# Performance work log

Measured on AMD Instinct MI355X. Metric: run time of the kernel, lower is better.

## Reference

```python
import jax, jax.numpy as jnp
import numpy as np

PI = 3.141592653589793

def _rel_transform(ent, rel):
    # ent: [E, d], rel: [E, d/2] (RotatE-style rotation composition)
    re, im = jnp.split(ent, 2, axis=-1)
    r = rel / (1.5 / PI)
    cr, sr = jnp.cos(r), jnp.sin(r)
    return jnp.concatenate([re * cr + im * sr, re * sr - im * cr], axis=-1)

def setup_inputs() -> dict:
    key = jax.random.key(0)
    ks = jax.random.split(key, 10)
    num_ent, d, num_rel, E2 = 100000, 128, 500, 1000000
    def kaiming(k, shape):
        fan_in = shape[1] if len(shape) > 1 else shape[0]
        return jax.random.normal(k, shape, jnp.float32) * np.sqrt(2.0 / fan_in)
    return {
        "x": jax.random.normal(ks[0], (num_ent, d), jnp.float32),
        "edge_index": jax.random.randint(ks[1], (2, E2), 0, num_ent),
        "edge_type": jax.random.randint(ks[2], (E2,), 0, num_rel),
        "rel_embed": jax.random.normal(ks[3], (num_rel, d // 2), jnp.float32),
        "w_loop": kaiming(ks[4], (d, d)),
        "w_in": kaiming(ks[5], (d, d)),
        "w_out": kaiming(ks[6], (d, d)),
        "w_rel": kaiming(ks[7], (d // 2, d // 2)),
        "loop_rel": kaiming(ks[8], (1, d // 2)),
    }

def reference(x, edge_index, edge_type, rel_embed, w_loop, w_in, w_out, w_rel, loop_rel):
    num_ent = x.shape[0]
    rel_all = jnp.concatenate([rel_embed, loop_rel], axis=0)  # [R+1, d/2]
    E = edge_index.shape[1] // 2
    in_idx, out_idx = edge_index[:, :E], edge_index[:, E:]
    in_type, out_type = edge_type[:E], edge_type[E:]

    def compute_norm(ei):
        row, col = ei[0], ei[1]
        deg = jnp.zeros((num_ent,), x.dtype).at[row].add(1.0)
        dinv = jnp.where(deg > 0, deg ** -0.5, 0.0)
        return dinv[row] * dinv[col]

    def propagate(ei, et, W, norm):
        x_j = x[ei[1]]                      # [E, d] edge gather
        msg = _rel_transform(x_j, rel_all[et]) @ W
        msg = msg * norm[:, None]
        return jnp.zeros((num_ent, W.shape[1]), x.dtype).at[ei[0]].add(msg)

    in_res = propagate(in_idx, in_type, w_in, compute_norm(in_idx))
    out_res = propagate(out_idx, out_type, w_out, compute_norm(out_idx))
    # self-loop: identity index scatter == elementwise, no norm
    loop_res = _rel_transform(x, jnp.broadcast_to(rel_all[-1], (num_ent, rel_all.shape[1]))) @ w_loop
    out = (in_res + out_res + loop_res) * (1.0 / 3.0)
    return out, (rel_all @ w_rel)[:-1]
```

## Files before the change

kernel.cpp:

```cpp
#include <hip/hip_runtime.h>
#include <hip/hip_bf16.h>
#include <math.h>

#define D 128
#define DH 64
#define CHUNK 2048
#define EPB 8
#define DEG_EPT 16
typedef __attribute__((ext_vector_type(8))) short bf16x8;
typedef __attribute__((ext_vector_type(4))) float f32x4;
constexpr float KREL = 3.141592653589793f / 1.5f;

static __device__ __forceinline__ unsigned short bf16u(float f) {
    return __builtin_bit_cast(unsigned short, __float2bfloat16(f));
}
static __device__ __forceinline__ unsigned packbf(float re, float im) {
    return (unsigned)bf16u(re) | ((unsigned)bf16u(im) << 16);
}

__global__ __launch_bounds__(256) void k_prelude(
    const float* __restrict__ x, const int* __restrict__ ei,
    const float* __restrict__ rel_embed, const float* __restrict__ loop_rel,
    const float* __restrict__ w_in, const float* __restrict__ w_out,
    const float* __restrict__ w_loop, const float* __restrict__ w_rel,
    int num_rel, int num_ent, int E2,
    int o1, int o2, int o3, int o4,
    unsigned* __restrict__ pt2, unsigned short* __restrict__ Bsw,
    float* __restrict__ out2, unsigned* __restrict__ xp,
    unsigned* __restrict__ deg, unsigned* __restrict__ rnk) {
    int b = blockIdx.x, tid = threadIdx.x;
    if (b < o1) {
        int base_e = b * (256 * DEG_EPT) + tid;
        int idxv[DEG_EPT]; unsigned rv[DEG_EPT]; bool ok[DEG_EPT];
#pragma unroll
        for (int q = 0; q < DEG_EPT; ++q) {
            int e = base_e + q * 256;
            ok[q] = (e < E2);
            int row = ok[q] ? ei[e] : 0;
            int h = (e < (E2 >> 1)) ? 0 : 1;
            idxv[q] = h * num_ent + row;
        }
#pragma unroll
        for (int q = 0; q < DEG_EPT; ++q)
            if (ok[q]) rv[q] = atomicAdd(&deg[idxv[q]], 1u);
#pragma unroll
        for (int q = 0; q < DEG_EPT; ++q) {
            int e = base_e + q * 256;
            if (ok[q]) rnk[e] = rv[q];
        }
    } else if (b < o2) {
        int i = (b - o1) * 256 + tid;
        if (i >= num_ent * 16) return;
        int row = i >> 4, q = i & 15;
        const float* xr = x + (size_t)row * D + q * 4;
        float4 re4 = *reinterpret_cast<const float4*>(xr);
        float4 im4 = *reinterpret_cast<const float4*>(xr + DH);
        uint4 o;
        o.x = packbf(re4.x, im4.x);
        o.y = packbf(re4.y, im4.y);
        o.z = packbf(re4.z, im4.z);
        o.w = packbf(re4.w, im4.w);
        reinterpret_cast<uint4*>(xp + (size_t)row * 64)[q] = o;
    } else if (b < o3) {
        int i = (b - o2) * 256 + tid;
        int total = (num_rel + 1) * DH;
        if (i >= total) return;
        int r = i / DH, c = i % DH;
        float v = (r < num_rel) ? rel_embed[r * DH + c] : loop_rel[c];
        float ang = v * KREL;
        pt2[i] = packbf(cosf(ang), sinf(ang));
    } else if (b < o4) {
        int i = (b - o3) * 256 + tid;
        int j = i & 7;
        int lane = (i >> 3) & 63;
        int fid = i >> 9;
        int ct = fid & 7;
        int kt = (fid >> 3) & 3;
        int plane = fid >> 5;
        int kp = kt * 32 + ((lane >> 4) << 3) + j;
        int orig = (kp >> 1) + (kp & 1) * DH;
        int col = ct * 16 + (lane & 15);
        float val;
        if (plane == 0) val = w_in[orig * 128 + col];
        else if (plane == 1) val = w_out[orig * 128 + col];
        else {
            int kk = orig & (DH - 1);
            float ang = loop_rel[kk] * KREL;
            float c = cosf(ang), s = sinf(ang);
            float w0 = w_loop[kk * 128 + col], w1 = w_loop[(DH + kk) * 128 + col];
            val = (orig < DH) ? fmaf(c, w0, s * w1) : (s * w0 - c * w1);
        }
        Bsw[i] = bf16u(val * (1.0f / 3.0f));
    } else {
        int i = (b - o4) * 256 + tid;
        if (i >= num_rel * DH) return;
        int r = i / DH, j = i % DH;
        const float* a = rel_embed + r * DH;
        float acc = 0.f;
#pragma unroll 8
        for (int k = 0; k < DH; ++k) acc = fmaf(a[k], w_rel[k * DH + j], acc);
        out2[i] = acc;
    }
}

__global__ void k_scan1(const unsigned* __restrict__ deg, int n,
                        unsigned* __restrict__ rp, unsigned* __restrict__ partials) {
    __shared__ unsigned s[256];
    int tid = threadIdx.x;
    int base = blockIdx.x * CHUNK + tid * 8;
    unsigned v[8]; unsigned sum = 0;
#pragma unroll
    for (int i = 0; i < 8; ++i) { int g = base + i; v[i] = (g < n) ? deg[g] : 0u; sum += v[i]; }
    s[tid] = sum; __syncthreads();
    for (int off = 1; off < 256; off <<= 1) {
        unsigned t = (tid >= off) ? s[tid - off] : 0u;
        __syncthreads();
        s[tid] += t;
        __syncthreads();
    }
    if (tid == 255) partials[blockIdx.x] = s[255];
    unsigned run = (tid ? s[tid - 1] : 0u);
#pragma unroll
    for (int i = 0; i < 8; ++i) { int g = base + i; if (g < n) rp[g] = run; run += v[i]; }
}

__global__ void k_scan2(unsigned* __restrict__ partials, int nb) {
    __shared__ unsigned s[256];
    int tid = threadIdx.x;
    unsigned v = (tid < nb) ? partials[tid] : 0u;
    s[tid] = v; __syncthreads();
    for (int off = 1; off < 256; off <<= 1) {
        unsigned t = (tid >= off) ? s[tid - off] : 0u;
        __syncthreads();
        s[tid] += t;
        __syncthreads();
    }
    if (tid < nb) partials[tid] = (tid ? s[tid - 1] : 0u);
}

__global__ void k_fill(const int* __restrict__ ei, const int* __restrict__ et,
                       int E2, int num_ent,
                       const unsigned* __restrict__ deg, const unsigned* __restrict__ rp,
                       const unsigned* __restrict__ partials,
                       const unsigned* __restrict__ rnk, int2* __restrict__ csr) {
    int e = blockIdx.x * blockDim.x + threadIdx.x;
    if (e >= E2) return;
    int Eh = E2 >> 1;
    int h = (e < Eh) ? 0 : 1;
    int row = ei[e], col = ei[E2 + e], t = et[e];
    int idx = h * num_ent + row;
    unsigned dr = deg[idx], dc = deg[h * num_ent + col];
    float nrm = (dr > 0u && dc > 0u) ? rsqrtf((float)dr * (float)dc) : 0.f;
    unsigned slot = rp[idx] + partials[idx >> 11] + rnk[e];
    unsigned meta = (unsigned)col | ((unsigned)t << 17) | ((unsigned)(idx & 15) << 26);
    csr[slot] = make_int2((int)meta, __float_as_int(nrm));
}

__global__ __launch_bounds__(256) void k_rowgather(
    const unsigned* __restrict__ xp, const int2* __restrict__ csr,
    const unsigned* __restrict__ rp, const unsigned* __restrict__ partials,
    const unsigned* __restrict__ deg, int E2, int n2,
    const unsigned* __restrict__ pt2, unsigned short* __restrict__ T2) {
    int gwave = (int)((blockIdx.x * 256u + threadIdx.x) >> 6);
    int lane = threadIdx.x & 63;
    int vr0 = gwave * 16;
    if (vr0 >= n2) return;
    int vlim = min(vr0 + 16, n2);
    int nrows = vlim - vr0;

    unsigned dv = (lane < nrows) ? deg[vr0 + lane] : 1u;
    unsigned long long zm = __ballot(lane < nrows && dv == 0u);
    while (zm) {
        int r = (int)(__ffsll((long long)zm) - 1);
        zm &= zm - 1;
        ((unsigned*)(T2 + (size_t)(vr0 + r) * D))[lane] = 0u;
    }

    unsigned beg = rp[vr0] + partials[vr0 >> 11];
    unsigned end = (vlim == n2) ? (unsigned)E2
                                : rp[vlim] + partials[vlim >> 11];
    if (beg >= end) return;

    const unsigned* xpl = xp + lane;
    const unsigned* ptl = pt2 + lane;

    int cur = -1;
    float a_re = 0.f, a_im = 0.f;

    auto loadbatch = [&](unsigned s) -> int2 {
        unsigned idx = s + (unsigned)(lane & 7);
        if (idx >= end) idx = end - 1;
        return csr[idx];
    };

    int2 mv = loadbatch(beg);
    for (unsigned s = beg; s < end; s += EPB) {
        int2 mvn = mv;
        if (s + EPB < end) mvn = loadbatch(s + EPB);
        int n = (int)min((unsigned)EPB, end - s);

        unsigned meta[EPB]; float nm[EPB];
        unsigned u[EPB], cu[EPB];
#pragma unroll
        for (int k = 0; k < EPB; ++k) {
            meta[k] = (unsigned)__builtin_amdgcn_readlane(mv.x, k);
            unsigned nrw = (unsigned)__builtin_amdgcn_readlane(mv.y, k);
            nm[k] = (k < n) ? __uint_as_float(nrw) : 0.f;
            u[k]  = xpl[(size_t)(meta[k] & 0x1FFFFu) * 64];
            cu[k] = ptl[(size_t)((meta[k] >> 17) & 0x1FFu) * 64];
        }
#pragma unroll
        for (int k = 0; k < EPB; ++k) {
            int lrow = (int)(meta[k] >> 26);
            if (lrow != cur) {
                if (cur >= 0)
                    ((unsigned*)(T2 + (size_t)(vr0 + cur) * D))[lane] = packbf(a_re, a_im);
                cur = lrow; a_re = a_im = 0.f;
            }
            float re = __uint_as_float(u[k] << 16);
            float im = __uint_as_float(u[k] & 0xFFFF0000u);
            float c  = __uint_as_float(cu[k] << 16);
            float sn = __uint_as_float(cu[k] & 0xFFFF0000u);
            float tre = fmaf(re, c, im * sn);
            float tim = fmaf(re, sn, -(im * c));
            a_re = fmaf(nm[k], tre, a_re);
            a_im = fmaf(nm[k], tim, a_im);
        }
        mv = mvn;
    }
    if (cur >= 0)
        ((unsigned*)(T2 + (size_t)(vr0 + cur) * D))[lane] = packbf(a_re, a_im);
}

__global__ __launch_bounds__(256) void k_combine(
    const unsigned short* __restrict__ T2, const unsigned short* __restrict__ XP,
    const unsigned short* __restrict__ Bsw,
    int num_ent, float* __restrict__ out) {
    int tid = threadIdx.x;
    int lane = tid & 63;
    int wid = tid >> 6;
    int base = blockIdx.x * 64 + wid * 16;
    int arow = base + (lane & 15);
    if (arow >= num_ent) arow = num_ent - 1;
    int khi = (lane >> 4) << 3;

    f32x4 acc[8];
    f32x4 zero = {0.f, 0.f, 0.f, 0.f};
#pragma unroll
    for (int i = 0; i < 8; ++i) acc[i] = zero;

    auto run_kt = [&](bf16x8 afrag, int fid_base) {
#pragma unroll
        for (int ct = 0; ct < 8; ++ct) {
            const unsigned short* bp = Bsw + (((size_t)fid_base * 8 + ct) << 9) + (lane << 3);
            bf16x8 bfrag = *reinterpret_cast<const bf16x8*>(bp);
            acc[ct] = __builtin_amdgcn_mfma_f32_16x16x32_bf16(afrag, bfrag, acc[ct], 0, 0, 0);
        }
    };

#pragma unroll
    for (int plane = 0; plane < 2; ++plane) {
        const unsigned short* Ab = T2 + ((size_t)plane * num_ent + arow) * D;
#pragma unroll
        for (int kt = 0; kt < 4; ++kt) {
            bf16x8 afrag = *reinterpret_cast<const bf16x8*>(Ab + kt * 32 + khi);
            run_kt(afrag, plane * 4 + kt);
        }
    }
    {
        const unsigned short* Xb = XP + (size_t)arow * D;
#pragma unroll
        for (int kt = 0; kt < 4; ++kt) {
            bf16x8 afrag = *reinterpret_cast<const bf16x8*>(Xb + kt * 32 + khi);
            run_kt(afrag, 8 + kt);
        }
    }
    int rbase = base + ((lane >> 4) << 2);
    int colb = lane & 15;
#pragma unroll
    for (int ct = 0; ct < 8; ++ct) {
#pragma unroll
        for (int jj = 0; jj < 4; ++jj) {
            int g = rbase + jj;
            if (g < num_ent) out[(size_t)g * D + ct * 16 + colb] = acc[ct][jj];
        }
    }
}

extern "C" void kernel_launch(void* const* d_in, const int* in_sizes, int n_in,
                              void* d_out, int out_size, void* d_ws, size_t ws_size,
                              hipStream_t stream) {
    const float* x         = (const float*)d_in[0];
    const int*   ei        = (const int*)d_in[1];
    const int*   et        = (const int*)d_in[2];
    const float* rel_embed = (const float*)d_in[3];
    const float* w_loop    = (const float*)d_in[4];
    const float* w_in      = (const float*)d_in[5];
    const float* w_out     = (const float*)d_in[6];
    const float* w_rel     = (const float*)d_in[7];
    const float* loop_rel  = (const float*)d_in[8];
    float* out = (float*)d_out;

    int num_ent = in_sizes[0] / D;
    int E2      = in_sizes[2];
    int num_rel = in_sizes[3] / DH;
    float* out2 = out + (size_t)num_ent * D;

    int n2 = 2 * num_ent;
    char* ws = (char*)d_ws;
    unsigned* deg = (unsigned*)ws;
    unsigned* rp  = deg + n2;
    unsigned* partials = rp + n2;
    unsigned* rnk = partials + 256;
    size_t off = (size_t)(2 * n2 + 256 + E2) * sizeof(unsigned);
    off = (off + 15) & ~(size_t)15;
    int2* csr = (int2*)(ws + off);
    unsigned* pt2 = (unsigned*)(csr + E2);
    unsigned short* Bsw = (unsigned short*)(pt2 + (size_t)(num_rel + 1) * DH);
    unsigned short* T2 = Bsw + (size_t)3 * 4 * 8 * 512;
    unsigned* xp = (unsigned*)(T2 + (size_t)n2 * D);

    hipMemsetAsync(deg, 0, (size_t)n2 * sizeof(unsigned), stream);

    int nb_deg = (E2 + 256 * DEG_EPT - 1) / (256 * DEG_EPT);
    int nb_xpk = (num_ent * 16 + 255) / 256;
    int nb_tab = ((num_rel + 1) * DH + 255) / 256;
    int nb_wsw = (3 * 4 * 8 * 512) / 256;
    int nb_rel = (num_rel * DH + 255) / 256;
    int o1 = nb_deg, o2 = o1 + nb_xpk, o3 = o2 + nb_tab, o4 = o3 + nb_wsw;
    int o5 = o4 + nb_rel;
    k_prelude<<<o5, 256, 0, stream>>>(x, ei, rel_embed, loop_rel,
                                      w_in, w_out, w_loop, w_rel,
                                      num_rel, num_ent, E2, o1, o2, o3, o4,
                                      pt2, Bsw, out2, xp, deg, rnk);

    int nb1 = (n2 + CHUNK - 1) / CHUNK;
    k_scan1<<<nb1, 256, 0, stream>>>(deg, n2, rp, partials);
    k_scan2<<<1, 256, 0, stream>>>(partials, nb1);

    k_fill<<<(E2 + 255) / 256, 256, 0, stream>>>(ei, et, E2, num_ent, deg, rp,
                                                 partials, rnk, csr);

    int nwaves = (n2 + 15) / 16;
    int gblocks = (nwaves * 64 + 255) / 256;
    k_rowgather<<<gblocks, 256, 0, stream>>>(xp, csr, rp, partials, deg,
                                             E2, n2, pt2, T2);

    int cb = (num_ent + 63) / 64;
    k_combine<<<cb, 256, 0, stream>>>(T2, (const unsigned short*)xp, Bsw, num_ent, out);
}
```

Before: 169.8 us.

## Replicate degree histogram across eight copies to reduce atomic contention

Degree-counting atomics are spread across eight replicated histograms chosen by block index. A new pass turns the per-replica counts into prefix offsets and writes the total degree. The CSR fill adds each edge's replica offset to compute its slot. This is meant to cut atomic contention, but it costs eight times the memset and more memory traffic, plus an extra kernel launch and scattered reads.

```diff
diff --git a/kernel.cpp b/kernel.cpp
--- a/kernel.cpp
+++ b/kernel.cpp
@@ -7,6 +7,7 @@
 #define CHUNK 2048
 #define EPB 8
 #define DEG_EPT 16
+#define NREP 8
 typedef __attribute__((ext_vector_type(8))) short bf16x8;
 typedef __attribute__((ext_vector_type(4))) float f32x4;
 constexpr float KREL = 3.141592653589793f / 1.5f;
@@ -27,9 +28,11 @@
     int o1, int o2, int o3, int o4,
     unsigned* __restrict__ pt2, unsigned short* __restrict__ Bsw,
     float* __restrict__ out2, unsigned* __restrict__ xp,
-    unsigned* __restrict__ deg, unsigned* __restrict__ rnk) {
+    unsigned* __restrict__ degR, unsigned* __restrict__ rnk) {
     int b = blockIdx.x, tid = threadIdx.x;
+    int n2 = 2 * num_ent;
     if (b < o1) {
+        unsigned* degrep = degR + (size_t)(b & (NREP - 1)) * n2;
         int base_e = b * (256 * DEG_EPT) + tid;
         int idxv[DEG_EPT]; unsigned rv[DEG_EPT]; bool ok[DEG_EPT];
 #pragma unroll
@@ -42,7 +45,7 @@
         }
 #pragma unroll
         for (int q = 0; q < DEG_EPT; ++q)
-            if (ok[q]) rv[q] = atomicAdd(&deg[idxv[q]], 1u);
+            if (ok[q]) rv[q] = atomicAdd(&degrep[idxv[q]], 1u);
 #pragma unroll
         for (int q = 0; q < DEG_EPT; ++q) {
             int e = base_e + q * 256;
@@ -103,6 +106,20 @@
     }
 }
 
+__global__ void k_scanR(unsigned* __restrict__ degR, unsigned* __restrict__ deg,
+                        int n2) {
+    int idx = blockIdx.x * blockDim.x + threadIdx.x;
+    if (idx >= n2) return;
+    unsigned run = 0;
+#pragma unroll
+    for (int r = 0; r < NREP; ++r) {
+        unsigned v = degR[(size_t)r * n2 + idx];
+        degR[(size_t)r * n2 + idx] = run;
+        run += v;
+    }
+    deg[idx] = run;
+}
+
 __global__ void k_scan1(const unsigned* __restrict__ deg, int n,
                         unsigned* __restrict__ rp, unsigned* __restrict__ partials) {
     __shared__ unsigned s[256];
@@ -142,16 +159,20 @@
                        int E2, int num_ent,
                        const unsigned* __restrict__ deg, const unsigned* __restrict__ rp,
                        const unsigned* __restrict__ partials,
+                       const unsigned* __restrict__ degR,
                        const unsigned* __restrict__ rnk, int2* __restrict__ csr) {
     int e = blockIdx.x * blockDim.x + threadIdx.x;
     if (e >= E2) return;
+    int n2 = 2 * num_ent;
     int Eh = E2 >> 1;
     int h = (e < Eh) ? 0 : 1;
     int row = ei[e], col = ei[E2 + e], t = et[e];
     int idx = h * num_ent + row;
     unsigned dr = deg[idx], dc = deg[h * num_ent + col];
     float nrm = (dr > 0u && dc > 0u) ? rsqrtf((float)dr * (float)dc) : 0.f;
-    unsigned slot = rp[idx] + partials[idx >> 11] + rnk[e];
+    int rep = (e >> 12) & (NREP - 1);
+    unsigned slot = rp[idx] + partials[idx >> 11]
+                  + degR[(size_t)rep * n2 + idx] + rnk[e];
     unsigned meta = (unsigned)col | ((unsigned)t << 17) | ((unsigned)(idx & 15) << 26);
     csr[slot] = make_int2((int)meta, __float_as_int(nrm));
 }
@@ -308,11 +329,12 @@
 
     int n2 = 2 * num_ent;
     char* ws = (char*)d_ws;
-    unsigned* deg = (unsigned*)ws;
-    unsigned* rp  = deg + n2;
+    unsigned* degR = (unsigned*)ws;
+    unsigned* deg  = degR + (size_t)NREP * n2;
+    unsigned* rp   = deg + n2;
     unsigned* partials = rp + n2;
     unsigned* rnk = partials + 256;
-    size_t off = (size_t)(2 * n2 + 256 + E2) * sizeof(unsigned);
+    size_t off = ((size_t)(NREP + 2) * n2 + 256 + E2) * sizeof(unsigned);
     off = (off + 15) & ~(size_t)15;
     int2* csr = (int2*)(ws + off);
     unsigned* pt2 = (unsigned*)(csr + E2);
@@ -320,7 +342,7 @@
     unsigned short* T2 = Bsw + (size_t)3 * 4 * 8 * 512;
     unsigned* xp = (unsigned*)(T2 + (size_t)n2 * D);
 
-    hipMemsetAsync(deg, 0, (size_t)n2 * sizeof(unsigned), stream);
+    hipMemsetAsync(degR, 0, (size_t)NREP * n2 * sizeof(unsigned), stream);
 
     int nb_deg = (E2 + 256 * DEG_EPT - 1) / (256 * DEG_EPT);
     int nb_xpk = (num_ent * 16 + 255) / 256;
@@ -332,14 +354,16 @@
     k_prelude<<<o5, 256, 0, stream>>>(x, ei, rel_embed, loop_rel,
                                       w_in, w_out, w_loop, w_rel,
                                       num_rel, num_ent, E2, o1, o2, o3, o4,
-                                      pt2, Bsw, out2, xp, deg, rnk);
+                                      pt2, Bsw, out2, xp, degR, rnk);
+
+    k_scanR<<<(n2 + 255) / 256, 256, 0, stream>>>(degR, deg, n2);
 
     int nb1 = (n2 + CHUNK - 1) / CHUNK;
     k_scan1<<<nb1, 256, 0, stream>>>(deg, n2, rp, partials);
     k_scan2<<<1, 256, 0, stream>>>(partials, nb1);
 
     k_fill<<<(E2 + 255) / 256, 256, 0, stream>>>(ei, et, E2, num_ent, deg, rp,
-                                                 partials, rnk, csr);
+                                                 partials, degR, rnk, csr);
 
     int nwaves = (n2 + 15) / 16;
     int gblocks = (nwaves * 64 + 255) / 256;
```

Result: slower. 183.6 us (+8.2%).
